# Optimization experiments

Measured on AMD Instinct MI355X. Metric: run time of the kernel, lower is better.

Reference implementation:

```python
import jax, jax.numpy as jnp
import numpy as np

D_MODEL = 1024
NUM_HEADS = 16
HEAD_DIM = D_MODEL // NUM_HEADS


def setup_inputs() -> dict:
    key = jax.random.key(0)
    ks = jax.random.split(key, 7)
    B, S = 2, 2048
    scale = 1.0 / np.sqrt(D_MODEL)
    inp = {
        "input": jax.random.normal(ks[0], (B, S, D_MODEL), dtype=jnp.float32),
        "W_q": jax.random.normal(ks[1], (D_MODEL, D_MODEL), dtype=jnp.float32) * scale,
        "b_q": jax.random.normal(ks[2], (D_MODEL,), dtype=jnp.float32) * 0.01,
        "W_k": jax.random.normal(ks[3], (D_MODEL, D_MODEL), dtype=jnp.float32) * scale,
        "b_k": jax.random.normal(ks[4], (D_MODEL,), dtype=jnp.float32) * 0.01,
        "W_v": jax.random.normal(ks[5], (D_MODEL, D_MODEL), dtype=jnp.float32) * scale,
        "b_v": jax.random.normal(ks[6], (D_MODEL,), dtype=jnp.float32) * 0.01,
    }
    return inp


def reference(input, W_q, b_q, W_k, b_k, W_v, b_v):
    B, S, _ = input.shape
    # QKV projections (torch nn.Linear: x @ W^T + b); split heads -> [B,H,S,Dh]
    def proj(W, b):
        y = jnp.einsum('bsd,ed->bse', input, W) + b
        return y.reshape(B, S, NUM_HEADS, HEAD_DIM).transpose(0, 2, 1, 3)

    Q = proj(W_q, b_q)
    K = proj(W_k, b_k)
    V = proj(W_v, b_v)

    scores = jnp.einsum('bhqd,bhkd->bhqk', Q, K) / jnp.sqrt(
        jnp.asarray(HEAD_DIM, dtype=input.dtype))
    attention_weights = jax.nn.softmax(scores, axis=-1)  # [B,H,S,S]
    out = jnp.einsum('bhqk,bhkd->bhqd', attention_weights, V)
    out = out.transpose(0, 2, 1, 3).reshape(B, S, D_MODEL)
    return out, attention_weights
```

## Files before the change

kernel.cpp:

```cpp
#include <hip/hip_runtime.h>
#include <stdint.h>

#define S_LEN   2048
#define D_MODEL 1024
#define N_HEADS 16
#define HEAD_D  64
#define BATCH   2
#define M_TOT   (BATCH * S_LEN)

typedef __attribute__((ext_vector_type(8))) short s8v;
typedef __attribute__((ext_vector_type(4))) float f4v;
typedef __attribute__((ext_vector_type(4))) unsigned short u4v;

__device__ __forceinline__ float bf2f(unsigned short u) {
    union { unsigned int i; float f; } c; c.i = ((unsigned int)u) << 16; return c.f;
}
__device__ __forceinline__ unsigned short f2bf(float f) {
    union { float f; unsigned int i; } c; c.f = f;
    unsigned int u = c.i + 0x7FFFu + ((c.i >> 16) & 1u);
    return (unsigned short)(u >> 16);
}
__device__ __forceinline__ unsigned int pk2bf(float lo, float hi) {
    return (unsigned int)f2bf(lo) | ((unsigned int)f2bf(hi) << 16);
}
__device__ __forceinline__ float hw_exp2(float x) { return __builtin_amdgcn_exp2f(x); }

#define GLD16(gp, lp) __builtin_amdgcn_global_load_lds(                      \
    (const __attribute__((address_space(1))) void*)(const void*)(gp),        \
    (__attribute__((address_space(3))) void*)(void*)(lp), 16, 0, 0)

#define BAR_LGKM() asm volatile("s_waitcnt lgkmcnt(0)\n\ts_barrier" ::: "memory")

#define EXP_SCALE 0.1803368801111204f

__global__ __launch_bounds__(256) void cvt_bf16(const float* __restrict__ src,
                                                unsigned short* __restrict__ dst, int n) {
    int i = (blockIdx.x * 256 + threadIdx.x) * 4;
    int stride = gridDim.x * 1024;
    for (; i < n; i += stride) {
        float4 v = *(const float4*)(src + i);
        u4v o;
        o[0] = f2bf(v.x); o[1] = f2bf(v.y); o[2] = f2bf(v.z); o[3] = f2bf(v.w);
        *(u4v*)(dst + i) = o;
    }
}

__global__ __launch_bounds__(256) void qkv_gemm(
    const unsigned short* __restrict__ X,
    const unsigned short* __restrict__ Wq, const unsigned short* __restrict__ Wk,
    const unsigned short* __restrict__ Wv,
    const float* __restrict__ bq, const float* __restrict__ bk, const float* __restrict__ bv,
    unsigned short* __restrict__ q_ws, unsigned short* __restrict__ k_ws,
    unsigned short* __restrict__ vt_ws) {
    __shared__ unsigned short sA[128 * 32];
    __shared__ unsigned short sB[128 * 32];

    const int z = blockIdx.z;
    const unsigned short* Wm = (z == 0) ? Wq : ((z == 1) ? Wk : Wv);
    const float* bm = (z == 0) ? bq : ((z == 1) ? bk : bv);
    const int m0 = blockIdx.x * 128, n0 = blockIdx.y * 128;
    const int t = threadIdx.x;
    const int lane = t & 63, w = t >> 6;
    const int fr = lane & 15, g = lane >> 4;
    const int wr = w >> 1, wc = w & 1;

    f4v acc[4][4];
#pragma unroll
    for (int i = 0; i < 4; ++i)
#pragma unroll
        for (int j = 0; j < 4; ++j) acc[i][j] = (f4v){0.f, 0.f, 0.f, 0.f};

    const int rowL = t >> 2;
    const int colL = (t & 3) * 8;
    const unsigned short* gA = X + (size_t)(m0 + rowL) * D_MODEL + colL;
    const unsigned short* gB = Wm + (size_t)(n0 + rowL) * D_MODEL + colL;

    for (int kb = 0; kb < 32; ++kb) {
        const int k0 = kb * 32;
        GLD16(gA + k0,                 sA + w * 512);
        GLD16(gA + 64 * D_MODEL + k0,  sA + 2048 + w * 512);
        GLD16(gB + k0,                 sB + w * 512);
        GLD16(gB + 64 * D_MODEL + k0,  sB + 2048 + w * 512);
        __syncthreads();

        s8v af[4], bfv[4];
#pragma unroll
        for (int i = 0; i < 4; ++i)
            af[i] = *(const s8v*)(sA + (wr * 64 + i * 16 + fr) * 32 + g * 8);
#pragma unroll
        for (int j = 0; j < 4; ++j)
            bfv[j] = *(const s8v*)(sB + (wc * 64 + j * 16 + fr) * 32 + g * 8);
#pragma unroll
        for (int i = 0; i < 4; ++i)
#pragma unroll
            for (int j = 0; j < 4; ++j)
                acc[i][j] = __builtin_amdgcn_mfma_f32_16x16x32_bf16(af[i], bfv[j], acc[i][j], 0, 0, 0);
        __syncthreads();
    }

    const int e_base = n0 + wc * 64;
    const int m_base = m0 + wr * 64;
    if (z < 2) {
        unsigned short* dst = (z == 0) ? q_ws : k_ws;
#pragma unroll
        for (int i = 0; i < 4; ++i) {
#pragma unroll
            for (int j = 0; j < 4; ++j) {
                const int e = e_base + j * 16 + fr;
                const int h = e >> 6, dh = e & 63;
                const float bias = bm[e];
                const int mr = m_base + i * 16 + g * 4;
                const int b_ = mr >> 11, srow = mr & 2047;
                const size_t base = (((size_t)(b_ * N_HEADS + h) * S_LEN + srow) << 6) + dh;
#pragma unroll
                for (int r = 0; r < 4; ++r)
                    dst[base + ((size_t)r << 6)] = f2bf(acc[i][j][r] + bias);
            }
        }
    } else {
#pragma unroll
        for (int i = 0; i < 4; ++i) {
#pragma unroll
            for (int j = 0; j < 4; ++j) {
                const int e = e_base + j * 16 + fr;
                const int h = e >> 6, dh = e & 63;
                const float bias = bm[e];
                const int mr = m_base + i * 16 + g * 4;
                const int b_ = mr >> 11, srow = mr & 2047;
                u4v pk;
#pragma unroll
                for (int r = 0; r < 4; ++r) pk[r] = f2bf(acc[i][j][r] + bias);
                *(u4v*)(vt_ws + ((size_t)(b_ * N_HEADS + h) * HEAD_D + dh) * S_LEN + srow) = pk;
            }
        }
    }
}

__global__ __launch_bounds__(256, 4) void attn_fused4(
    const unsigned short* __restrict__ q_ws, const unsigned short* __restrict__ k_ws,
    const unsigned short* __restrict__ vt_ws,
    float* __restrict__ out, float* __restrict__ wts) {
    __shared__ unsigned short KL[2][4096];
    __shared__ unsigned short VL[2][4096];
    __shared__ unsigned short PLb[4][1024];

    const int t = threadIdx.x, lane = t & 63, w = t >> 6;
    const int fr = lane & 15, g = lane >> 4;
    const int blk = blockIdx.x;
    const int bh = (blk & 7) * 4 + (blk >> 8);
    const int qt = (blk >> 3) & 31;

    const unsigned short* Qp = q_ws + ((size_t)bh * S_LEN + qt * 64 + w * 16) * HEAD_D;
    const unsigned short* Kp = k_ws + (size_t)bh * S_LEN * HEAD_D;
    const unsigned short* Vt = vt_ws + (size_t)bh * HEAD_D * S_LEN;

    const s8v qa0 = *(const s8v*)(Qp + fr * HEAD_D + g * 8);
    const s8v qa1 = *(const s8v*)(Qp + fr * HEAD_D + 32 + g * 8);

    auto stageK = [&](int c, int buf) {
#pragma unroll
        for (int j = 0; j < 2; ++j) {
            const int d = t * 16 + j * 4096;
            const int row = d >> 7, cb = (d >> 4) & 7;
            GLD16(Kp + (size_t)(c * 64 + row) * HEAD_D + ((cb ^ (row & 7)) << 3),
                  &KL[buf][w * 512 + j * 2048]);
        }
    };
    auto stageV = [&](int c, int buf) {
#pragma unroll
        for (int j = 0; j < 2; ++j) {
            const int d = t * 16 + j * 4096;
            const int row = d >> 7, cb = (d >> 4) & 7;
            GLD16(Vt + (size_t)row * S_LEN + c * 64 + ((cb ^ (row & 7)) << 3),
                  &VL[buf][w * 512 + j * 2048]);
        }
    };
    auto qk16 = [&](const unsigned short* kb, int st) -> f4v {
        const int row = st * 16 + fr, m = row & 7;
        const s8v ka0 = *(const s8v*)((const char*)kb + row * 128 + ((g ^ m) << 4));
        const s8v ka1 = *(const s8v*)((const char*)kb + row * 128 + (((4 + g) ^ m) << 4));
        f4v s = (f4v){0.f, 0.f, 0.f, 0.f};
        s = __builtin_amdgcn_mfma_f32_16x16x32_bf16(ka0, qa0, s, 0, 0, 0);
        s = __builtin_amdgcn_mfma_f32_16x16x32_bf16(ka1, qa1, s, 0, 0, 0);
        return s;
    };

    float rsum = 0.f;
    stageK(0, 0);
    for (int c = 0; c < 32; ++c) {
        const int cur = c & 1;
        if (c < 31) stageK(c + 1, cur ^ 1);
        if (c < 31) asm volatile("s_waitcnt vmcnt(2)" ::: "memory");
        else        asm volatile("s_waitcnt vmcnt(0)" ::: "memory");
        asm volatile("s_barrier" ::: "memory");
        const unsigned short* kb = KL[cur];
#pragma unroll
        for (int st = 0; st < 4; ++st) {
            const f4v s = qk16(kb, st);
#pragma unroll
            for (int r = 0; r < 4; ++r) rsum += hw_exp2(s[r] * EXP_SCALE);
        }
        BAR_LGKM();
    }
    rsum += __shfl_xor(rsum, 16);
    rsum += __shfl_xor(rsum, 32);
    const float inv = 1.f / rsum;

    f4v acc[4];
#pragma unroll
    for (int i = 0; i < 4; ++i) acc[i] = (f4v){0.f, 0.f, 0.f, 0.f};
    unsigned short* PL = PLb[w];
    const int swp = (fr & 7) << 4;
    float* wbase = wts + ((size_t)bh * S_LEN + qt * 64 + w * 16) * S_LEN;

    stageK(0, 0); stageV(0, 0);
    for (int c = 0; c < 32; ++c) {
        const int cur = c & 1;
        if (c < 31) { stageK(c + 1, cur ^ 1); stageV(c + 1, cur ^ 1); }
        if (c == 0)      asm volatile("s_waitcnt vmcnt(4)" ::: "memory");
        else if (c < 31) asm volatile("s_waitcnt vmcnt(8)" ::: "memory");
        else             asm volatile("s_waitcnt vmcnt(4)" ::: "memory");
        asm volatile("s_barrier" ::: "memory");

        const unsigned short* kb = KL[cur];
#pragma unroll
        for (int st = 0; st < 4; ++st) {
            const f4v s = qk16(kb, st);
            f4v p;
#pragma unroll
            for (int r = 0; r < 4; ++r) p[r] = hw_exp2(s[r] * EXP_SCALE) * inv;
            const int base = fr * 128 + st * 32 + g * 8;
            *(unsigned int*)((char*)PL + ((base)     ^ swp)) = pk2bf(p[0], p[1]);
            *(unsigned int*)((char*)PL + ((base + 4) ^ swp)) = pk2bf(p[2], p[3]);
        }

        {
            const int r0 = lane >> 4, cc = lane & 15;
#pragma unroll
            for (int i = 0; i < 4; ++i) {
                const int row = i * 4 + r0;
                const u4v pw = *(const u4v*)((const char*)PL +
                                             ((row * 128 + cc * 8) ^ ((row & 7) << 4)));
                f4v o;
#pragma unroll
                for (int e = 0; e < 4; ++e) o[e] = bf2f(pw[e]);
                __builtin_nontemporal_store(o,
                    (f4v*)(wbase + (size_t)row * S_LEN + c * 64 + cc * 4));
            }
        }

        const char* vl = (const char*)VL[cur];
#pragma unroll
        for (int ks = 0; ks < 2; ++ks) {
            const s8v pa = *(const s8v*)((const char*)PL +
                                         ((fr * 128 + ks * 64 + g * 16) ^ swp));
#pragma unroll
            for (int tt = 0; tt < 4; ++tt) {
                const int vrow = tt * 16 + fr;
                const s8v vv = *(const s8v*)(vl + vrow * 128 +
                                             (((ks * 4 + g) ^ (vrow & 7)) << 4));
                acc[tt] = __builtin_amdgcn_mfma_f32_16x16x32_bf16(pa, vv, acc[tt], 0, 0, 0);
            }
        }
        BAR_LGKM();
    }

    const int b_ = bh >> 4, h = bh & 15;
#pragma unroll
    for (int tt = 0; tt < 4; ++tt)
#pragma unroll
        for (int r = 0; r < 4; ++r)
            __builtin_nontemporal_store(acc[tt][r],
                &out[((size_t)b_ * S_LEN + qt * 64 + w * 16 + g * 4 + r) * D_MODEL +
                     h * HEAD_D + tt * 16 + fr]);
}

extern "C" void kernel_launch(void* const* d_in, const int* in_sizes, int n_in,
                              void* d_out, int out_size, void* d_ws, size_t ws_size,
                              hipStream_t stream) {
    const float* x  = (const float*)d_in[0];
    const float* Wq = (const float*)d_in[1];
    const float* bq = (const float*)d_in[2];
    const float* Wk = (const float*)d_in[3];
    const float* bk = (const float*)d_in[4];
    const float* Wv = (const float*)d_in[5];
    const float* bv = (const float*)d_in[6];

    float* out = (float*)d_out;
    float* wts = out + (size_t)BATCH * S_LEN * D_MODEL;

    unsigned short* xb    = (unsigned short*)d_ws;
    unsigned short* wqb   = xb  + (size_t)M_TOT * D_MODEL;
    unsigned short* wkb   = wqb + (size_t)D_MODEL * D_MODEL;
    unsigned short* wvb   = wkb + (size_t)D_MODEL * D_MODEL;
    unsigned short* q_ws  = wvb + (size_t)D_MODEL * D_MODEL;
    unsigned short* k_ws  = q_ws + (size_t)M_TOT * D_MODEL;
    unsigned short* vt_ws = k_ws + (size_t)M_TOT * D_MODEL;

    cvt_bf16<<<1024, 256, 0, stream>>>(x,  xb,  M_TOT * D_MODEL);
    cvt_bf16<<<256,  256, 0, stream>>>(Wq, wqb, D_MODEL * D_MODEL);
    cvt_bf16<<<256,  256, 0, stream>>>(Wk, wkb, D_MODEL * D_MODEL);
    cvt_bf16<<<256,  256, 0, stream>>>(Wv, wvb, D_MODEL * D_MODEL);

    qkv_gemm<<<dim3(32, 8, 3), 256, 0, stream>>>(xb, wqb, wkb, wvb, bq, bk, bv,
                                                 q_ws, k_ws, vt_ws);

    attn_fused4<<<BATCH * N_HEADS * (S_LEN / 64), 256, 0, stream>>>(q_ws, k_ws, vt_ws, out, wts);
}
```

Baseline: 207.1 us.

## Merge LDS buffers, widen row-sum K tiles, store fp32 weights directly

Replaces the separate K, V and P shared arrays with one unioned 40KB LDS region. The first pass, which only computes row sums, now stages 128-key K tiles and so runs half as many loop iterations and barriers. The weight output is now written straight from the fp32 probabilities in the MFMA layout, instead of being re-read from the bf16 P tile in LDS and widened. This removes a round trip through LDS and the bf16 rounding of stored weights. In exchange the global stores become less coalesced: each lane writes 16 bytes scattered across rows rather than contiguous row segments.

```diff
diff --git a/kernel.cpp b/kernel.cpp
--- a/kernel.cpp
+++ b/kernel.cpp
@@ -136,13 +136,11 @@
     }
 }
 
-__global__ __launch_bounds__(256, 4) void attn_fused4(
+__global__ __launch_bounds__(256, 4) void attn_fused5(
     const unsigned short* __restrict__ q_ws, const unsigned short* __restrict__ k_ws,
     const unsigned short* __restrict__ vt_ws,
     float* __restrict__ out, float* __restrict__ wts) {
-    __shared__ unsigned short KL[2][4096];
-    __shared__ unsigned short VL[2][4096];
-    __shared__ unsigned short PLb[4][1024];
+    __shared__ __align__(16) char SM[40960];
 
     const int t = threadIdx.x, lane = t & 63, w = t >> 6;
     const int fr = lane & 15, g = lane >> 4;
@@ -157,28 +155,37 @@
     const s8v qa0 = *(const s8v*)(Qp + fr * HEAD_D + g * 8);
     const s8v qa1 = *(const s8v*)(Qp + fr * HEAD_D + 32 + g * 8);
 
-    auto stageK = [&](int c, int buf) {
+    auto stageK64 = [&](int c, char* dst) {
 #pragma unroll
         for (int j = 0; j < 2; ++j) {
             const int d = t * 16 + j * 4096;
             const int row = d >> 7, cb = (d >> 4) & 7;
             GLD16(Kp + (size_t)(c * 64 + row) * HEAD_D + ((cb ^ (row & 7)) << 3),
-                  &KL[buf][w * 512 + j * 2048]);
+                  dst + w * 1024 + j * 4096);
         }
     };
-    auto stageV = [&](int c, int buf) {
+    auto stageV64 = [&](int c, char* dst) {
 #pragma unroll
         for (int j = 0; j < 2; ++j) {
             const int d = t * 16 + j * 4096;
             const int row = d >> 7, cb = (d >> 4) & 7;
             GLD16(Vt + (size_t)row * S_LEN + c * 64 + ((cb ^ (row & 7)) << 3),
-                  &VL[buf][w * 512 + j * 2048]);
+                  dst + w * 1024 + j * 4096);
         }
     };
-    auto qk16 = [&](const unsigned short* kb, int st) -> f4v {
+    auto stageK128 = [&](int c, char* dst) {
+#pragma unroll
+        for (int j = 0; j < 4; ++j) {
+            const int d = t * 16 + j * 4096;
+            const int row = d >> 7, cb = (d >> 4) & 7;
+            GLD16(Kp + (size_t)(c * 128 + row) * HEAD_D + ((cb ^ (row & 7)) << 3),
+                  dst + w * 1024 + j * 4096);
+        }
+    };
+    auto qk16 = [&](const char* kb, int st) -> f4v {
         const int row = st * 16 + fr, m = row & 7;
-        const s8v ka0 = *(const s8v*)((const char*)kb + row * 128 + ((g ^ m) << 4));
-        const s8v ka1 = *(const s8v*)((const char*)kb + row * 128 + (((4 + g) ^ m) << 4));
+        const s8v ka0 = *(const s8v*)(kb + row * 128 + ((g ^ m) << 4));
+        const s8v ka1 = *(const s8v*)(kb + row * 128 + (((4 + g) ^ m) << 4));
         f4v s = (f4v){0.f, 0.f, 0.f, 0.f};
         s = __builtin_amdgcn_mfma_f32_16x16x32_bf16(ka0, qa0, s, 0, 0, 0);
         s = __builtin_amdgcn_mfma_f32_16x16x32_bf16(ka1, qa1, s, 0, 0, 0);
@@ -186,16 +193,16 @@
     };
 
     float rsum = 0.f;
-    stageK(0, 0);
-    for (int c = 0; c < 32; ++c) {
+    stageK128(0, SM);
+    for (int c = 0; c < 16; ++c) {
         const int cur = c & 1;
-        if (c < 31) stageK(c + 1, cur ^ 1);
-        if (c < 31) asm volatile("s_waitcnt vmcnt(2)" ::: "memory");
+        if (c < 15) stageK128(c + 1, SM + (cur ^ 1) * 16384);
+        if (c < 15) asm volatile("s_waitcnt vmcnt(4)" ::: "memory");
         else        asm volatile("s_waitcnt vmcnt(0)" ::: "memory");
         asm volatile("s_barrier" ::: "memory");
-        const unsigned short* kb = KL[cur];
-#pragma unroll
-        for (int st = 0; st < 4; ++st) {
+        const char* kb = SM + cur * 16384;
+#pragma unroll
+        for (int st = 0; st < 8; ++st) {
             const f4v s = qk16(kb, st);
 #pragma unroll
             for (int r = 0; r < 4; ++r) rsum += hw_exp2(s[r] * EXP_SCALE);
@@ -209,47 +216,35 @@
     f4v acc[4];
 #pragma unroll
     for (int i = 0; i < 4; ++i) acc[i] = (f4v){0.f, 0.f, 0.f, 0.f};
-    unsigned short* PL = PLb[w];
+    unsigned short* PL = (unsigned short*)(SM + 32768 + w * 2048);
     const int swp = (fr & 7) << 4;
     float* wbase = wts + ((size_t)bh * S_LEN + qt * 64 + w * 16) * S_LEN;
 
-    stageK(0, 0); stageV(0, 0);
+    stageK64(0, SM); stageV64(0, SM + 16384);
     for (int c = 0; c < 32; ++c) {
         const int cur = c & 1;
-        if (c < 31) { stageK(c + 1, cur ^ 1); stageV(c + 1, cur ^ 1); }
+        if (c < 31) { stageK64(c + 1, SM + (cur ^ 1) * 8192);
+                      stageV64(c + 1, SM + 16384 + (cur ^ 1) * 8192); }
         if (c == 0)      asm volatile("s_waitcnt vmcnt(4)" ::: "memory");
         else if (c < 31) asm volatile("s_waitcnt vmcnt(8)" ::: "memory");
         else             asm volatile("s_waitcnt vmcnt(4)" ::: "memory");
         asm volatile("s_barrier" ::: "memory");
 
-        const unsigned short* kb = KL[cur];
+        const char* kb = SM + cur * 8192;
 #pragma unroll
         for (int st = 0; st < 4; ++st) {
             const f4v s = qk16(kb, st);
             f4v p;
 #pragma unroll
             for (int r = 0; r < 4; ++r) p[r] = hw_exp2(s[r] * EXP_SCALE) * inv;
+            __builtin_nontemporal_store(p,
+                (f4v*)(wbase + (size_t)fr * S_LEN + c * 64 + st * 16 + g * 4));
             const int base = fr * 128 + st * 32 + g * 8;
             *(unsigned int*)((char*)PL + ((base)     ^ swp)) = pk2bf(p[0], p[1]);
             *(unsigned int*)((char*)PL + ((base + 4) ^ swp)) = pk2bf(p[2], p[3]);
         }
 
-        {
-            const int r0 = lane >> 4, cc = lane & 15;
-#pragma unroll
-            for (int i = 0; i < 4; ++i) {
-                const int row = i * 4 + r0;
-                const u4v pw = *(const u4v*)((const char*)PL +
-                                             ((row * 128 + cc * 8) ^ ((row & 7) << 4)));
-                f4v o;
-#pragma unroll
-                for (int e = 0; e < 4; ++e) o[e] = bf2f(pw[e]);
-                __builtin_nontemporal_store(o,
-                    (f4v*)(wbase + (size_t)row * S_LEN + c * 64 + cc * 4));
-            }
-        }
-
-        const char* vl = (const char*)VL[cur];
+        const char* vl = SM + 16384 + cur * 8192;
 #pragma unroll
         for (int ks = 0; ks < 2; ++ks) {
             const s8v pa = *(const s8v*)((const char*)PL +
@@ -305,5 +300,5 @@
     qkv_gemm<<<dim3(32, 8, 3), 256, 0, stream>>>(xb, wqb, wkb, wvb, bq, bk, bv,
                                                  q_ws, k_ws, vt_ws);
 
-    attn_fused4<<<BATCH * N_HEADS * (S_LEN / 64), 256, 0, stream>>>(q_ws, k_ws, vt_ws, out, wts);
-}
+    attn_fused5<<<BATCH * N_HEADS * (S_LEN / 64), 256, 0, stream>>>(q_ws, k_ws, vt_ws, out, wts);
+}
```

Result: slower. 250.0 us (+20.7%).
